# Optimization experiments

Hardware: AMD Instinct MI355X
Metric: run time of the kernel (lower is better)

## Reference

```python
import jax, jax.numpy as jnp
import numpy as np

S, B, H, F, E, K = 2048, 4, 1024, 4096, 8, 2


def setup_inputs() -> dict:
    key = jax.random.key(0)
    k1, k2, k3, k4 = jax.random.split(key, 4)
    scale_h = 1.0 / np.sqrt(H)
    scale_f = 1.0 / np.sqrt(F)
    return {
        "x": jax.random.normal(k1, (S, B, H), dtype=jnp.float32),
        "router_w": jax.random.normal(k2, (H, E), dtype=jnp.float32) * scale_h,
        "w1": jax.random.normal(k3, (E, H, F), dtype=jnp.float32) * scale_h,
        "w2": jax.random.normal(k4, (E, F, H), dtype=jnp.float32) * scale_f,
    }


def reference(x, router_w, w1, w2):
    # x: [S, B, H] (Megatron layout). Flatten to tokens.
    s, b, h = x.shape
    xt = x.reshape(-1, h)                       # [T, H], T = S*B
    # --- TopK router: softmax over expert logits, then top-k probs ---
    logits = xt @ router_w                      # [T, E]
    probs = jax.nn.softmax(logits, axis=-1)     # [T, E]
    top_p, top_i = jax.lax.top_k(probs, K)      # [T, K] each
    # --- Grouped-GEMM expert MLPs + weighted combine ---
    # Loop over the small fixed expert set; each expert applies fc1->gelu->fc2
    # to every token, masked/weighted by its routing probability (math is
    # identical to dispatch/permute/grouped-GEMM/combine in Megatron).
    out = jnp.zeros_like(xt)
    for e in range(E):
        gate_e = jnp.sum(jnp.where(top_i == e, top_p, 0.0), axis=-1)  # [T]
        hidden = jax.nn.gelu(xt @ w1[e], approximate=True)            # [T, F]
        out = out + gate_e[:, None] * (hidden @ w2[e])                # [T, H]
    return out.reshape(s, b, h)
```

## Files before the change

### kernel.cpp

```cpp
#include <hip/hip_runtime.h>
#include <cstdint>
#include <cstddef>

#define T_TOKENS 8192
#define H_DIM    1024
#define F_DIM    4096
#define E_NUM    8

typedef __bf16 bf16x8 __attribute__((ext_vector_type(8)));
typedef float  f32x4  __attribute__((ext_vector_type(4)));
typedef unsigned short ushort8 __attribute__((ext_vector_type(8)));

#define AS_GLOBAL(p) ((const __attribute__((address_space(1))) void*)(p))
#define AS_LDS(p)    ((__attribute__((address_space(3))) void*)(p))

__device__ inline unsigned short f2b(float f) {
  unsigned int u = __float_as_uint(f);
  unsigned int r = (u + 0x7fffu + ((u >> 16) & 1u)) >> 16;
  return (unsigned short)r;
}
__device__ inline float b2f(unsigned short u) {
  return __uint_as_float(((unsigned int)u) << 16);
}
__device__ inline float gelu_fast(float v) {
  float u2 = 1.5957691216057308f * v * (1.0f + 0.044715f * v * v);
  return v / (1.0f + __expf(-u2));
}

__global__ __launch_bounds__(256) void transpose_cast_kernel(
    const float* __restrict__ in, unsigned short* __restrict__ out, int R, int C)
{
  __shared__ float tile[64][65];
  const int e  = blockIdx.z;
  const int c0 = blockIdx.x * 64;
  const int r0 = blockIdx.y * 64;
  const float* src = in + (size_t)e * R * C;
  unsigned short* dst = out + (size_t)e * R * C;
  const int tid = threadIdx.x;
  const int rl  = tid >> 4;
  const int cl4 = (tid & 15) * 4;
#pragma unroll
  for (int i = 0; i < 4; ++i) {
    float4 v = *(const float4*)(src + (size_t)(r0 + rl + i * 16) * C + c0 + cl4);
    tile[rl + i * 16][cl4 + 0] = v.x;
    tile[rl + i * 16][cl4 + 1] = v.y;
    tile[rl + i * 16][cl4 + 2] = v.z;
    tile[rl + i * 16][cl4 + 3] = v.w;
  }
  __syncthreads();
  const int cl = tid >> 2;
  const int rb = (tid & 3) * 16;
#pragma unroll
  for (int j = 0; j < 4; ++j) {
    ushort4 u;
    u.x = f2b(tile[rb + j * 4 + 0][cl]);
    u.y = f2b(tile[rb + j * 4 + 1][cl]);
    u.z = f2b(tile[rb + j * 4 + 2][cl]);
    u.w = f2b(tile[rb + j * 4 + 3][cl]);
    *(ushort4*)(dst + (size_t)(c0 + cl) * R + r0 + rb + j * 4) = u;
  }
}

__global__ void zero_meta_kernel(int* __restrict__ counts) {
  if (threadIdx.x < 24) counts[threadIdx.x] = 0;
}

__global__ __launch_bounds__(256) void router_kernel(
    const float* __restrict__ x, const float* __restrict__ rw,
    unsigned short* __restrict__ xb, int* __restrict__ top_e, float* __restrict__ top_p,
    int* __restrict__ counts)
{
  __shared__ float lrw[H_DIM * 9];
  __shared__ int lc[E_NUM];
  const int tid = threadIdx.x;
  if (tid < E_NUM) lc[tid] = 0;
  for (int r = tid; r < H_DIM; r += 256) {
    const float* s = rw + r * 8;
    float4 a = *(const float4*)(s);
    float4 b = *(const float4*)(s + 4);
    float* d = &lrw[r * 9];
    d[0] = a.x; d[1] = a.y; d[2] = a.z; d[3] = a.w;
    d[4] = b.x; d[5] = b.y; d[6] = b.z; d[7] = b.w;
  }
  __syncthreads();
  const int lane = tid & 63, wid = tid >> 6;
  for (int i = 0; i < 8; ++i) {
    const int t = blockIdx.x * 32 + wid * 8 + i;
    float acc[8] = {0.f, 0.f, 0.f, 0.f, 0.f, 0.f, 0.f, 0.f};
    const float* xrow = x + (size_t)t * H_DIM;
    unsigned short* xbrow = xb + (size_t)t * H_DIM;
#pragma unroll
    for (int j = 0; j < 16; ++j) {
      int h = j * 64 + lane;
      float xv = xrow[h];
      xbrow[h] = f2b(xv);
      const float* rr = &lrw[h * 9];
#pragma unroll
      for (int e = 0; e < 8; ++e) acc[e] += xv * rr[e];
    }
#pragma unroll
    for (int e = 0; e < 8; ++e) {
#pragma unroll
      for (int s = 32; s > 0; s >>= 1) acc[e] += __shfl_xor(acc[e], s, 64);
    }
    if (lane == 0) {
      float mx = acc[0];
      for (int e = 1; e < 8; ++e) mx = fmaxf(mx, acc[e]);
      float p[8]; float sum = 0.f;
      for (int e = 0; e < 8; ++e) { p[e] = expf(acc[e] - mx); sum += p[e]; }
      float inv = 1.0f / sum;
      int i1 = 0; float b1 = p[0];
      for (int e = 1; e < 8; ++e) if (p[e] > b1) { b1 = p[e]; i1 = e; }
      int i2 = (i1 == 0) ? 1 : 0; float b2 = p[i2];
      for (int e = 0; e < 8; ++e) if (e != i1 && p[e] > b2) { b2 = p[e]; i2 = e; }
      top_e[2 * t]     = i1; top_p[2 * t]     = b1 * inv;
      top_e[2 * t + 1] = i2; top_p[2 * t + 1] = b2 * inv;
      atomicAdd(&lc[i1], 1);
      atomicAdd(&lc[i2], 1);
    }
  }
  __syncthreads();
  if (tid < E_NUM) atomicAdd(&counts[tid], lc[tid]);
}

__global__ void offsets_kernel(const int* __restrict__ counts,
                               int* __restrict__ offsets, int* __restrict__ cursor) {
  if (threadIdx.x == 0) {
    int o = 0;
    for (int e = 0; e < E_NUM; ++e) { offsets[e] = o; o += counts[e]; cursor[e] = 0; }
  }
}

__global__ __launch_bounds__(256) void assign_kernel(
    const int* __restrict__ top_e, const float* __restrict__ top_p,
    const int* __restrict__ offsets, int* __restrict__ cursor,
    int* __restrict__ map, float* __restrict__ gate, int* __restrict__ slot_of)
{
  __shared__ int lc[E_NUM], lb[E_NUM];
  const int tid = threadIdx.x;
  const int t = blockIdx.x * 256 + tid;
  if (tid < E_NUM) lc[tid] = 0;
  __syncthreads();
  int e0 = top_e[2 * t], e1 = top_e[2 * t + 1];
  int p0 = atomicAdd(&lc[e0], 1);
  int p1 = atomicAdd(&lc[e1], 1);
  __syncthreads();
  if (tid < E_NUM) lb[tid] = atomicAdd(&cursor[tid], lc[tid]);
  __syncthreads();
  int s0 = offsets[e0] + lb[e0] + p0;
  int s1 = offsets[e1] + lb[e1] + p1;
  map[s0] = t; gate[s0] = top_p[2 * t];
  map[s1] = t; gate[s1] = top_p[2 * t + 1];
  slot_of[2 * t] = s0; slot_of[2 * t + 1] = s1;
}

template <int KD, int ND, bool USE_MAP, bool GELU>
__global__ __launch_bounds__(256) void moe_gemm_kernel(
    const unsigned short* __restrict__ A, const unsigned short* __restrict__ Bt,
    const int* __restrict__ map, const float* __restrict__ gate,
    const int* __restrict__ counts, const int* __restrict__ offsets,
    unsigned short* __restrict__ C)
{
  __shared__ unsigned short ls[32768];
  const int e   = blockIdx.x;
  const int cnt = counts[e];
  const int tile_m = blockIdx.y;
  if (tile_m * 128 >= cnt) return;
  const int off    = offsets[e];
  const int tile_n = blockIdx.z;
  const int tid    = threadIdx.x;

  const unsigned short* aSrc[4];
  const unsigned short* bSrc[4];
  const int cswz = ((tid & 7) ^ ((tid >> 3) & 7)) * 8;
#pragma unroll
  for (int it = 0; it < 4; ++it) {
    int r  = it * 32 + (tid >> 3);
    int rm = tile_m * 128 + r;
    if (rm > cnt - 1) rm = cnt - 1;
    int arow = USE_MAP ? map[off + rm] : (off + rm);
    aSrc[it] = A + (size_t)arow * KD + cswz;
    int rn = tile_n * 128 + r;
    bSrc[it] = Bt + (size_t)e * ND * KD + (size_t)rn * KD + cswz;
  }

  const int lane = tid & 63;
  const int wid  = tid >> 6;
  const int wm = wid >> 1, wn = wid & 1;
  const int lr = lane & 15, kg = lane >> 4;
  const int swz = lr & 7;

  f32x4 acc[4][4];
#pragma unroll
  for (int mi = 0; mi < 4; ++mi)
#pragma unroll
    for (int ni = 0; ni < 4; ++ni) acc[mi][ni] = (f32x4){0.f, 0.f, 0.f, 0.f};

  constexpr int NK = KD / 64;

#pragma unroll
  for (int it = 0; it < 4; ++it)
    __builtin_amdgcn_global_load_lds(AS_GLOBAL(aSrc[it]),
                                     AS_LDS(ls + (it * 256 + tid) * 8), 16, 0, 0);
#pragma unroll
  for (int it = 0; it < 4; ++it)
    __builtin_amdgcn_global_load_lds(AS_GLOBAL(bSrc[it]),
                                     AS_LDS(ls + 16384 + (it * 256 + tid) * 8), 16, 0, 0);

#pragma unroll 1
  for (int k = 0; k < NK; ++k) {
    const int p = k & 1;
    asm volatile("s_barrier" ::: "memory");
    if (k + 1 < NK) {
      const int q = p ^ 1;
      const int k0 = (k + 1) * 64;
#pragma unroll
      for (int it = 0; it < 4; ++it)
        __builtin_amdgcn_global_load_lds(AS_GLOBAL(aSrc[it] + k0),
                                         AS_LDS(ls + q * 8192 + (it * 256 + tid) * 8), 16, 0, 0);
#pragma unroll
      for (int it = 0; it < 4; ++it)
        __builtin_amdgcn_global_load_lds(AS_GLOBAL(bSrc[it] + k0),
                                         AS_LDS(ls + 16384 + q * 8192 + (it * 256 + tid) * 8), 16, 0, 0);
      asm volatile("s_waitcnt vmcnt(8)" ::: "memory");
    } else {
      asm volatile("s_waitcnt vmcnt(0)" ::: "memory");
    }
    asm volatile("s_barrier" ::: "memory");

    const unsigned short* pA = ls + p * 8192 + (wm * 64 + lr) * 64;
    const unsigned short* pB = ls + 16384 + p * 8192 + (wn * 64 + lr) * 64;
#pragma unroll
    for (int ks = 0; ks < 2; ++ks) {
      bf16x8 aF[4], bF[4];
#pragma unroll
      for (int i = 0; i < 4; ++i)
        aF[i] = *(const bf16x8*)(pA + i * 16 * 64 + (((ks * 4 + kg) ^ swz) * 8));
#pragma unroll
      for (int i = 0; i < 4; ++i)
        bF[i] = *(const bf16x8*)(pB + i * 16 * 64 + (((ks * 4 + kg) ^ swz) * 8));
#pragma unroll
      for (int mi = 0; mi < 4; ++mi)
#pragma unroll
        for (int ni = 0; ni < 4; ++ni)
          acc[mi][ni] = __builtin_amdgcn_mfma_f32_16x16x32_bf16(aF[mi], bF[ni],
                                                                acc[mi][ni], 0, 0, 0);
    }
  }

  __syncthreads();
#pragma unroll
  for (int mi = 0; mi < 4; ++mi) {
#pragma unroll
    for (int r = 0; r < 4; ++r) {
      int Rl = wm * 64 + mi * 16 + kg * 4 + r;
      float gv = 1.0f;
      if (!GELU) {
        int gm = tile_m * 128 + Rl;
        int gmc = gm < cnt ? gm : cnt - 1;
        gv = gate[off + gmc];
      }
#pragma unroll
      for (int ni = 0; ni < 4; ++ni) {
        int col = wn * 64 + ni * 16 + lr;
        float v = acc[mi][ni][r];
        v = GELU ? gelu_fast(v) : v * gv;
        ls[Rl * 136 + col] = f2b(v);
      }
    }
  }
  __syncthreads();
#pragma unroll
  for (int it = 0; it < 8; ++it) {
    int g = it * 256 + tid;
    int R = g >> 4, c16 = g & 15;
    int gm = tile_m * 128 + R;
    if (gm < cnt) {
      ushort8 v = *(const ushort8*)(ls + R * 136 + c16 * 8);
      *(ushort8*)(C + (size_t)(off + gm) * ND + tile_n * 128 + c16 * 8) = v;
    }
  }
}

__global__ __launch_bounds__(256) void combine_kernel(
    const unsigned short* __restrict__ y, const int* __restrict__ slot_of,
    float* __restrict__ out)
{
  const int t  = blockIdx.x;
  const int h0 = threadIdx.x * 4;
  const int s0 = slot_of[2 * t], s1 = slot_of[2 * t + 1];
  ushort4 a = *(const ushort4*)(y + (size_t)s0 * H_DIM + h0);
  ushort4 b = *(const ushort4*)(y + (size_t)s1 * H_DIM + h0);
  float4 o;
  o.x = b2f(a.x) + b2f(b.x);
  o.y = b2f(a.y) + b2f(b.y);
  o.z = b2f(a.z) + b2f(b.z);
  o.w = b2f(a.w) + b2f(b.w);
  *(float4*)(out + (size_t)t * H_DIM + h0) = o;
}

extern "C" void kernel_launch(void* const* d_in, const int* in_sizes, int n_in,
                              void* d_out, int out_size, void* d_ws, size_t ws_size,
                              hipStream_t stream) {
  const float* x  = (const float*)d_in[0];
  const float* rw = (const float*)d_in[1];
  const float* w1 = (const float*)d_in[2];
  const float* w2 = (const float*)d_in[3];
  float* out = (float*)d_out;

  char* ws = (char*)d_ws;
  unsigned short* wT     = (unsigned short*)ws;
  unsigned short* xb     = (unsigned short*)(ws + (64ull  << 20));
  unsigned short* y      = (unsigned short*)(ws + (64ull  << 20));
  unsigned short* hidden = (unsigned short*)(ws + (96ull  << 20));
  char* meta = ws + (224ull << 20);
  int*   top_e   = (int*)meta;
  float* top_p   = (float*)(meta + (64 << 10));
  int*   map     = (int*)(meta + (128 << 10));
  float* gate    = (float*)(meta + (192 << 10));
  int*   slot_of = (int*)(meta + (256 << 10));
  int*   counts  = (int*)(meta + (320 << 10));
  int*   offsets = counts + 8;
  int*   cursor  = counts + 16;

  zero_meta_kernel<<<1, 64, 0, stream>>>(counts);
  transpose_cast_kernel<<<dim3(F_DIM / 64, H_DIM / 64, E_NUM), 256, 0, stream>>>(w1, wT, H_DIM, F_DIM);
  router_kernel<<<256, 256, 0, stream>>>(x, rw, xb, top_e, top_p, counts);
  offsets_kernel<<<1, 64, 0, stream>>>(counts, offsets, cursor);
  assign_kernel<<<T_TOKENS / 256, 256, 0, stream>>>(top_e, top_p, offsets, cursor, map, gate, slot_of);
  moe_gemm_kernel<H_DIM, F_DIM, true, true>
      <<<dim3(E_NUM, 64, F_DIM / 128), 256, 0, stream>>>(xb, wT, map, nullptr, counts, offsets, hidden);
  transpose_cast_kernel<<<dim3(H_DIM / 64, F_DIM / 64, E_NUM), 256, 0, stream>>>(w2, wT, F_DIM, H_DIM);
  moe_gemm_kernel<F_DIM, H_DIM, false, false>
      <<<dim3(E_NUM, 64, H_DIM / 128), 256, 0, stream>>>(hidden, wT, nullptr, gate, counts, offsets, y);
  combine_kernel<<<T_TOKENS, 256, 0, stream>>>(y, slot_of, out);
}
```

Before: 753.7 us.

## Add 256x256-tile 512-thread grouped GEMM for fc1 and widen transpose stores

Adds a new grouped GEMM kernel with 256x256 output tiles, 8 waves and double-buffered global-to-LDS loads, with priority hints around the MFMA phases. It is used only for the fc1 expert GEMM, to raise arithmetic intensity and cut reloads of the A and B tiles. Separately, the weight transpose-cast kernel now writes 8 bf16 values per store instead of 4. The larger tiles use much more LDS and many more accumulator registers, which lowers occupancy and wastes more padded rows when an expert's token count is not a multiple of 256.

```diff
diff --git a/kernel.cpp b/kernel.cpp
--- a/kernel.cpp
+++ b/kernel.cpp
@@ -48,16 +48,15 @@
     tile[rl + i * 16][cl4 + 3] = v.w;
   }
   __syncthreads();
-  const int cl = tid >> 2;
-  const int rb = (tid & 3) * 16;
-#pragma unroll
-  for (int j = 0; j < 4; ++j) {
-    ushort4 u;
-    u.x = f2b(tile[rb + j * 4 + 0][cl]);
-    u.y = f2b(tile[rb + j * 4 + 1][cl]);
-    u.z = f2b(tile[rb + j * 4 + 2][cl]);
-    u.w = f2b(tile[rb + j * 4 + 3][cl]);
-    *(ushort4*)(dst + (size_t)(c0 + cl) * R + r0 + rb + j * 4) = u;
+#pragma unroll
+  for (int itw = 0; itw < 2; ++itw) {
+    int g  = itw * 256 + tid;
+    int c  = g >> 3;
+    int rc = g & 7;
+    ushort8 u;
+#pragma unroll
+    for (int k = 0; k < 8; ++k) u[k] = f2b(tile[rc * 8 + k][c]);
+    *(ushort8*)(dst + (size_t)(c0 + c) * R + r0 + rc * 8) = u;
   }
 }
 
@@ -155,6 +154,178 @@
 }
 
 template <int KD, int ND, bool USE_MAP, bool GELU>
+__global__ __launch_bounds__(512, 2) void moe_gemm256_kernel(
+    const unsigned short* __restrict__ A, const unsigned short* __restrict__ Bt,
+    const int* __restrict__ map, const float* __restrict__ gate,
+    const int* __restrict__ counts, const int* __restrict__ offsets,
+    unsigned short* __restrict__ C)
+{
+  __shared__ unsigned short ls[65536];
+  const int e   = blockIdx.x;
+  const int cnt = counts[e];
+  const int tile_m = blockIdx.y;
+  if (tile_m * 256 >= cnt) return;
+  const int off    = offsets[e];
+  const int tile_n = blockIdx.z;
+  const int tid    = threadIdx.x;
+
+  const unsigned short* aSrc[4];
+  const unsigned short* bSrc[4];
+#pragma unroll
+  for (int it = 0; it < 4; ++it) {
+    int g   = it * 512 + tid;
+    int row = g >> 3;
+    int cs  = (g & 7) ^ (row & 7);
+    int rm  = tile_m * 256 + row;
+    if (rm > cnt - 1) rm = cnt - 1;
+    int arow = USE_MAP ? map[off + rm] : (off + rm);
+    aSrc[it] = A + (size_t)arow * KD + cs * 8;
+    int rn = tile_n * 256 + row;
+    bSrc[it] = Bt + (size_t)e * ND * KD + (size_t)rn * KD + cs * 8;
+  }
+
+  const int lane = tid & 63;
+  const int wid  = tid >> 6;
+  const int wm = wid >> 2, wn = wid & 3;
+  const int lr = lane & 15, kg = lane >> 4;
+  const int swz = lr & 7;
+
+  f32x4 acc[8][4];
+#pragma unroll
+  for (int mi = 0; mi < 8; ++mi)
+#pragma unroll
+    for (int ni = 0; ni < 4; ++ni) acc[mi][ni] = (f32x4){0.f, 0.f, 0.f, 0.f};
+
+  constexpr int NK = KD / 64;
+
+  auto STAGE = [&](int kt, int slot) {
+    const int kof = kt * 64;
+#pragma unroll
+    for (int it = 0; it < 4; ++it)
+      __builtin_amdgcn_global_load_lds(AS_GLOBAL(aSrc[it] + kof),
+          AS_LDS(ls + slot * 16384 + (it * 512 + tid) * 8), 16, 0, 0);
+#pragma unroll
+    for (int it = 0; it < 4; ++it)
+      __builtin_amdgcn_global_load_lds(AS_GLOBAL(bSrc[it] + kof),
+          AS_LDS(ls + 32768 + slot * 16384 + (it * 512 + tid) * 8), 16, 0, 0);
+  };
+
+  STAGE(0, 0);
+  STAGE(1, 1);
+  asm volatile("s_waitcnt vmcnt(8)" ::: "memory");
+  asm volatile("s_barrier" ::: "memory");
+
+#pragma unroll 1
+  for (int kt = 0; kt < NK; ++kt) {
+    const int s = kt & 1;
+    const unsigned short* pA = ls + s * 16384 + (wm * 128 + lr) * 64;
+    const unsigned short* pB = ls + 32768 + s * 16384 + (wn * 64 + lr) * 64;
+    bf16x8 aF[4], bF[4];
+
+#pragma unroll
+    for (int ni = 0; ni < 4; ++ni)
+      bF[ni] = *(const bf16x8*)(pB + ni * 16 * 64 + ((kg) ^ swz) * 8);
+#pragma unroll
+    for (int j = 0; j < 4; ++j)
+      aF[j] = *(const bf16x8*)(pA + j * 16 * 64 + ((kg) ^ swz) * 8);
+    asm volatile("s_barrier" ::: "memory");
+    __builtin_amdgcn_s_setprio(1);
+#pragma unroll
+    for (int j = 0; j < 4; ++j)
+#pragma unroll
+      for (int ni = 0; ni < 4; ++ni)
+        acc[j][ni] = __builtin_amdgcn_mfma_f32_16x16x32_bf16(aF[j], bF[ni], acc[j][ni], 0, 0, 0);
+    __builtin_amdgcn_s_setprio(0);
+
+#pragma unroll
+    for (int j = 0; j < 4; ++j)
+      aF[j] = *(const bf16x8*)(pA + (4 + j) * 16 * 64 + ((kg) ^ swz) * 8);
+    asm volatile("s_barrier" ::: "memory");
+    __builtin_amdgcn_s_setprio(1);
+#pragma unroll
+    for (int j = 0; j < 4; ++j)
+#pragma unroll
+      for (int ni = 0; ni < 4; ++ni)
+        acc[4 + j][ni] = __builtin_amdgcn_mfma_f32_16x16x32_bf16(aF[j], bF[ni], acc[4 + j][ni], 0, 0, 0);
+    __builtin_amdgcn_s_setprio(0);
+
+#pragma unroll
+    for (int ni = 0; ni < 4; ++ni)
+      bF[ni] = *(const bf16x8*)(pB + ni * 16 * 64 + ((4 + kg) ^ swz) * 8);
+#pragma unroll
+    for (int j = 0; j < 4; ++j)
+      aF[j] = *(const bf16x8*)(pA + j * 16 * 64 + ((4 + kg) ^ swz) * 8);
+    asm volatile("s_barrier" ::: "memory");
+    __builtin_amdgcn_s_setprio(1);
+#pragma unroll
+    for (int j = 0; j < 4; ++j)
+#pragma unroll
+      for (int ni = 0; ni < 4; ++ni)
+        acc[j][ni] = __builtin_amdgcn_mfma_f32_16x16x32_bf16(aF[j], bF[ni], acc[j][ni], 0, 0, 0);
+    __builtin_amdgcn_s_setprio(0);
+
+#pragma unroll
+    for (int j = 0; j < 4; ++j)
+      aF[j] = *(const bf16x8*)(pA + (4 + j) * 16 * 64 + ((4 + kg) ^ swz) * 8);
+    asm volatile("s_waitcnt lgkmcnt(0)" ::: "memory");
+    asm volatile("s_barrier" ::: "memory");
+    if (kt + 2 < NK) STAGE(kt + 2, s);
+    __builtin_amdgcn_s_setprio(1);
+#pragma unroll
+    for (int j = 0; j < 4; ++j)
+#pragma unroll
+      for (int ni = 0; ni < 4; ++ni)
+        acc[4 + j][ni] = __builtin_amdgcn_mfma_f32_16x16x32_bf16(aF[j], bF[ni], acc[4 + j][ni], 0, 0, 0);
+    __builtin_amdgcn_s_setprio(0);
+    if (kt + 2 < NK) {
+      asm volatile("s_waitcnt vmcnt(8)" ::: "memory");
+    } else {
+      asm volatile("s_waitcnt vmcnt(0)" ::: "memory");
+    }
+    asm volatile("s_barrier" ::: "memory");
+  }
+
+  __syncthreads();
+#pragma unroll
+  for (int h = 0; h < 2; ++h) {
+    if (h) __syncthreads();
+    if (wm == h) {
+#pragma unroll
+      for (int mi = 0; mi < 8; ++mi) {
+#pragma unroll
+        for (int r = 0; r < 4; ++r) {
+          int Rl = mi * 16 + kg * 4 + r;
+          float gv = 1.0f;
+          if (!GELU) {
+            int gm = tile_m * 256 + h * 128 + Rl;
+            int gmc = gm < cnt ? gm : cnt - 1;
+            gv = gate[off + gmc];
+          }
+#pragma unroll
+          for (int ni = 0; ni < 4; ++ni) {
+            int col = wn * 64 + ni * 16 + lr;
+            float v = acc[mi][ni][r];
+            v = GELU ? gelu_fast(v) : v * gv;
+            ls[Rl * 264 + col] = f2b(v);
+          }
+        }
+      }
+    }
+    __syncthreads();
+#pragma unroll
+    for (int it = 0; it < 8; ++it) {
+      int g = it * 512 + tid;
+      int R = g >> 5, c8 = g & 31;
+      int gm = tile_m * 256 + h * 128 + R;
+      if (gm < cnt) {
+        ushort8 v = *(const ushort8*)(ls + R * 264 + c8 * 8);
+        *(ushort8*)(C + (size_t)(off + gm) * ND + tile_n * 256 + c8 * 8) = v;
+      }
+    }
+  }
+}
+
+template <int KD, int ND, bool USE_MAP, bool GELU>
 __global__ __launch_bounds__(256) void moe_gemm_kernel(
     const unsigned short* __restrict__ A, const unsigned short* __restrict__ Bt,
     const int* __restrict__ map, const float* __restrict__ gate,
@@ -328,8 +499,8 @@
   router_kernel<<<256, 256, 0, stream>>>(x, rw, xb, top_e, top_p, counts);
   offsets_kernel<<<1, 64, 0, stream>>>(counts, offsets, cursor);
   assign_kernel<<<T_TOKENS / 256, 256, 0, stream>>>(top_e, top_p, offsets, cursor, map, gate, slot_of);
-  moe_gemm_kernel<H_DIM, F_DIM, true, true>
-      <<<dim3(E_NUM, 64, F_DIM / 128), 256, 0, stream>>>(xb, wT, map, nullptr, counts, offsets, hidden);
+  moe_gemm256_kernel<H_DIM, F_DIM, true, true>
+      <<<dim3(E_NUM, 32, F_DIM / 256), 512, 0, stream>>>(xb, wT, map, nullptr, counts, offsets, hidden);
   transpose_cast_kernel<<<dim3(H_DIM / 64, F_DIM / 64, E_NUM), 256, 0, stream>>>(w2, wT, F_DIM, H_DIM);
   moe_gemm_kernel<F_DIM, H_DIM, false, false>
       <<<dim3(E_NUM, 64, H_DIM / 128), 256, 0, stream>>>(hidden, wT, nullptr, gate, counts, offsets, y);
```

After: 796.9 us. 5.7% more time.

## Fuse combine into second GEMM via atomics and fold small setup kernels

Applied to the files above, without the earlier changes.

The second expert GEMM now scales its accumulators by the gate and atomically adds them in fp32 straight into the output rows, using the token map. This removes the bf16 intermediate y buffer and the separate combine kernel. To support this, the router kernel zeroes the output, the first transpose zeroes the counters, and assign computes the expert offsets itself, which drops two tiny launches. The transpose also writes 8-wide stores. In exchange the code relies on many scattered fp32 atomics and an extra full-size zeroing pass over the output.

```diff
diff --git a/kernel.cpp b/kernel.cpp
--- a/kernel.cpp
+++ b/kernel.cpp
@@ -28,15 +28,18 @@
 }
 
 __global__ __launch_bounds__(256) void transpose_cast_kernel(
-    const float* __restrict__ in, unsigned short* __restrict__ out, int R, int C)
+    const float* __restrict__ in, unsigned short* __restrict__ out, int R, int C,
+    int* __restrict__ zc)
 {
   __shared__ float tile[64][65];
+  const int tid = threadIdx.x;
+  if (zc && blockIdx.x == 0 && blockIdx.y == 0 && blockIdx.z == 0 && tid < 24)
+    zc[tid] = 0;
   const int e  = blockIdx.z;
   const int c0 = blockIdx.x * 64;
   const int r0 = blockIdx.y * 64;
   const float* src = in + (size_t)e * R * C;
   unsigned short* dst = out + (size_t)e * R * C;
-  const int tid = threadIdx.x;
   const int rl  = tid >> 4;
   const int cl4 = (tid & 15) * 4;
 #pragma unroll
@@ -48,31 +51,33 @@
     tile[rl + i * 16][cl4 + 3] = v.w;
   }
   __syncthreads();
-  const int cl = tid >> 2;
-  const int rb = (tid & 3) * 16;
-#pragma unroll
-  for (int j = 0; j < 4; ++j) {
-    ushort4 u;
-    u.x = f2b(tile[rb + j * 4 + 0][cl]);
-    u.y = f2b(tile[rb + j * 4 + 1][cl]);
-    u.z = f2b(tile[rb + j * 4 + 2][cl]);
-    u.w = f2b(tile[rb + j * 4 + 3][cl]);
-    *(ushort4*)(dst + (size_t)(c0 + cl) * R + r0 + rb + j * 4) = u;
-  }
-}
-
-__global__ void zero_meta_kernel(int* __restrict__ counts) {
-  if (threadIdx.x < 24) counts[threadIdx.x] = 0;
+#pragma unroll
+  for (int itw = 0; itw < 2; ++itw) {
+    int g  = itw * 256 + tid;
+    int c  = g >> 3;
+    int rc = g & 7;
+    ushort8 u;
+#pragma unroll
+    for (int k = 0; k < 8; ++k) u[k] = f2b(tile[rc * 8 + k][c]);
+    *(ushort8*)(dst + (size_t)(c0 + c) * R + r0 + rc * 8) = u;
+  }
 }
 
 __global__ __launch_bounds__(256) void router_kernel(
     const float* __restrict__ x, const float* __restrict__ rw,
     unsigned short* __restrict__ xb, int* __restrict__ top_e, float* __restrict__ top_p,
-    int* __restrict__ counts)
+    int* __restrict__ counts, float* __restrict__ out_zero)
 {
   __shared__ float lrw[H_DIM * 9];
   __shared__ int lc[E_NUM];
   const int tid = threadIdx.x;
+  {
+    float4 z = {0.f, 0.f, 0.f, 0.f};
+    float4* o4 = (float4*)out_zero;
+    int base = blockIdx.x * 256 + tid;
+#pragma unroll
+    for (int i = 0; i < 32; ++i) o4[base + i * 65536] = z;
+  }
   if (tid < E_NUM) lc[tid] = 0;
   for (int r = tid; r < H_DIM; r += 256) {
     const float* s = rw + r * 8;
@@ -123,23 +128,19 @@
   if (tid < E_NUM) atomicAdd(&counts[tid], lc[tid]);
 }
 
-__global__ void offsets_kernel(const int* __restrict__ counts,
-                               int* __restrict__ offsets, int* __restrict__ cursor) {
-  if (threadIdx.x == 0) {
-    int o = 0;
-    for (int e = 0; e < E_NUM; ++e) { offsets[e] = o; o += counts[e]; cursor[e] = 0; }
-  }
-}
-
 __global__ __launch_bounds__(256) void assign_kernel(
     const int* __restrict__ top_e, const float* __restrict__ top_p,
-    const int* __restrict__ offsets, int* __restrict__ cursor,
-    int* __restrict__ map, float* __restrict__ gate, int* __restrict__ slot_of)
+    const int* __restrict__ counts, int* __restrict__ cursor,
+    int* __restrict__ map, float* __restrict__ gate, int* __restrict__ offsets)
 {
-  __shared__ int lc[E_NUM], lb[E_NUM];
+  __shared__ int lc[E_NUM], lb[E_NUM], loff[E_NUM];
   const int tid = threadIdx.x;
   const int t = blockIdx.x * 256 + tid;
   if (tid < E_NUM) lc[tid] = 0;
+  if (tid == 0) {
+    int o = 0;
+    for (int e = 0; e < E_NUM; ++e) { loff[e] = o; o += counts[e]; }
+  }
   __syncthreads();
   int e0 = top_e[2 * t], e1 = top_e[2 * t + 1];
   int p0 = atomicAdd(&lc[e0], 1);
@@ -147,19 +148,19 @@
   __syncthreads();
   if (tid < E_NUM) lb[tid] = atomicAdd(&cursor[tid], lc[tid]);
   __syncthreads();
-  int s0 = offsets[e0] + lb[e0] + p0;
-  int s1 = offsets[e1] + lb[e1] + p1;
+  int s0 = loff[e0] + lb[e0] + p0;
+  int s1 = loff[e1] + lb[e1] + p1;
   map[s0] = t; gate[s0] = top_p[2 * t];
   map[s1] = t; gate[s1] = top_p[2 * t + 1];
-  slot_of[2 * t] = s0; slot_of[2 * t + 1] = s1;
-}
-
-template <int KD, int ND, bool USE_MAP, bool GELU>
+  if (blockIdx.x == 0 && tid < E_NUM) offsets[tid] = loff[tid];
+}
+
+template <int KD, int ND, bool USE_MAP, bool GELU, bool ATOMIC_OUT>
 __global__ __launch_bounds__(256) void moe_gemm_kernel(
     const unsigned short* __restrict__ A, const unsigned short* __restrict__ Bt,
     const int* __restrict__ map, const float* __restrict__ gate,
     const int* __restrict__ counts, const int* __restrict__ offsets,
-    unsigned short* __restrict__ C)
+    unsigned short* __restrict__ C, float* __restrict__ out)
 {
   __shared__ unsigned short ls[32768];
   const int e   = blockIdx.x;
@@ -248,55 +249,52 @@
     }
   }
 
-  __syncthreads();
-#pragma unroll
-  for (int mi = 0; mi < 4; ++mi) {
-#pragma unroll
-    for (int r = 0; r < 4; ++r) {
-      int Rl = wm * 64 + mi * 16 + kg * 4 + r;
-      float gv = 1.0f;
-      if (!GELU) {
+  if (ATOMIC_OUT) {
+#pragma unroll
+    for (int mi = 0; mi < 4; ++mi) {
+#pragma unroll
+      for (int r = 0; r < 4; ++r) {
+        int Rl = wm * 64 + mi * 16 + kg * 4 + r;
         int gm = tile_m * 128 + Rl;
-        int gmc = gm < cnt ? gm : cnt - 1;
-        gv = gate[off + gmc];
+        if (gm < cnt) {
+          int   t  = map[off + gm];
+          float gv = gate[off + gm];
+          float* orow = out + (size_t)t * ND + tile_n * 128 + wn * 64 + lr;
+#pragma unroll
+          for (int ni = 0; ni < 4; ++ni)
+            __hip_atomic_fetch_add(orow + ni * 16, acc[mi][ni][r] * gv,
+                                   __ATOMIC_RELAXED, __HIP_MEMORY_SCOPE_AGENT);
+        }
       }
-#pragma unroll
-      for (int ni = 0; ni < 4; ++ni) {
-        int col = wn * 64 + ni * 16 + lr;
-        float v = acc[mi][ni][r];
-        v = GELU ? gelu_fast(v) : v * gv;
-        ls[Rl * 136 + col] = f2b(v);
+    }
+  } else {
+    __syncthreads();
+#pragma unroll
+    for (int mi = 0; mi < 4; ++mi) {
+#pragma unroll
+      for (int r = 0; r < 4; ++r) {
+        int Rl = wm * 64 + mi * 16 + kg * 4 + r;
+#pragma unroll
+        for (int ni = 0; ni < 4; ++ni) {
+          int col = wn * 64 + ni * 16 + lr;
+          float v = acc[mi][ni][r];
+          v = GELU ? gelu_fast(v) : v;
+          ls[Rl * 136 + col] = f2b(v);
+        }
       }
     }
-  }
-  __syncthreads();
-#pragma unroll
-  for (int it = 0; it < 8; ++it) {
-    int g = it * 256 + tid;
-    int R = g >> 4, c16 = g & 15;
-    int gm = tile_m * 128 + R;
-    if (gm < cnt) {
-      ushort8 v = *(const ushort8*)(ls + R * 136 + c16 * 8);
-      *(ushort8*)(C + (size_t)(off + gm) * ND + tile_n * 128 + c16 * 8) = v;
-    }
-  }
-}
-
-__global__ __launch_bounds__(256) void combine_kernel(
-    const unsigned short* __restrict__ y, const int* __restrict__ slot_of,
-    float* __restrict__ out)
-{
-  const int t  = blockIdx.x;
-  const int h0 = threadIdx.x * 4;
-  const int s0 = slot_of[2 * t], s1 = slot_of[2 * t + 1];
-  ushort4 a = *(const ushort4*)(y + (size_t)s0 * H_DIM + h0);
-  ushort4 b = *(const ushort4*)(y + (size_t)s1 * H_DIM + h0);
-  float4 o;
-  o.x = b2f(a.x) + b2f(b.x);
-  o.y = b2f(a.y) + b2f(b.y);
-  o.z = b2f(a.z) + b2f(b.z);
-  o.w = b2f(a.w) + b2f(b.w);
-  *(float4*)(out + (size_t)t * H_DIM + h0) = o;
+    __syncthreads();
+#pragma unroll
+    for (int it = 0; it < 8; ++it) {
+      int g = it * 256 + tid;
+      int R = g >> 4, c16 = g & 15;
+      int gm = tile_m * 128 + R;
+      if (gm < cnt) {
+        ushort8 v = *(const ushort8*)(ls + R * 136 + c16 * 8);
+        *(ushort8*)(C + (size_t)(off + gm) * ND + tile_n * 128 + c16 * 8) = v;
+      }
+    }
+  }
 }
 
 extern "C" void kernel_launch(void* const* d_in, const int* in_sizes, int n_in,
@@ -311,27 +309,27 @@
   char* ws = (char*)d_ws;
   unsigned short* wT     = (unsigned short*)ws;
   unsigned short* xb     = (unsigned short*)(ws + (64ull  << 20));
-  unsigned short* y      = (unsigned short*)(ws + (64ull  << 20));
   unsigned short* hidden = (unsigned short*)(ws + (96ull  << 20));
   char* meta = ws + (224ull << 20);
   int*   top_e   = (int*)meta;
   float* top_p   = (float*)(meta + (64 << 10));
   int*   map     = (int*)(meta + (128 << 10));
   float* gate    = (float*)(meta + (192 << 10));
-  int*   slot_of = (int*)(meta + (256 << 10));
   int*   counts  = (int*)(meta + (320 << 10));
   int*   offsets = counts + 8;
   int*   cursor  = counts + 16;
 
-  zero_meta_kernel<<<1, 64, 0, stream>>>(counts);
-  transpose_cast_kernel<<<dim3(F_DIM / 64, H_DIM / 64, E_NUM), 256, 0, stream>>>(w1, wT, H_DIM, F_DIM);
-  router_kernel<<<256, 256, 0, stream>>>(x, rw, xb, top_e, top_p, counts);
-  offsets_kernel<<<1, 64, 0, stream>>>(counts, offsets, cursor);
-  assign_kernel<<<T_TOKENS / 256, 256, 0, stream>>>(top_e, top_p, offsets, cursor, map, gate, slot_of);
-  moe_gemm_kernel<H_DIM, F_DIM, true, true>
-      <<<dim3(E_NUM, 64, F_DIM / 128), 256, 0, stream>>>(xb, wT, map, nullptr, counts, offsets, hidden);
-  transpose_cast_kernel<<<dim3(H_DIM / 64, F_DIM / 64, E_NUM), 256, 0, stream>>>(w2, wT, F_DIM, H_DIM);
-  moe_gemm_kernel<F_DIM, H_DIM, false, false>
-      <<<dim3(E_NUM, 64, H_DIM / 128), 256, 0, stream>>>(hidden, wT, nullptr, gate, counts, offsets, y);
-  combine_kernel<<<T_TOKENS, 256, 0, stream>>>(y, slot_of, out);
-}
+  transpose_cast_kernel<<<dim3(F_DIM / 64, H_DIM / 64, E_NUM), 256, 0, stream>>>(
+      w1, wT, H_DIM, F_DIM, counts);
+  router_kernel<<<256, 256, 0, stream>>>(x, rw, xb, top_e, top_p, counts, out);
+  assign_kernel<<<T_TOKENS / 256, 256, 0, stream>>>(top_e, top_p, counts, cursor,
+                                                    map, gate, offsets);
+  moe_gemm_kernel<H_DIM, F_DIM, true, true, false>
+      <<<dim3(E_NUM, 64, F_DIM / 128), 256, 0, stream>>>(xb, wT, map, gate,
+                                                         counts, offsets, hidden, nullptr);
+  transpose_cast_kernel<<<dim3(H_DIM / 64, F_DIM / 64, E_NUM), 256, 0, stream>>>(
+      w2, wT, F_DIM, H_DIM, nullptr);
+  moe_gemm_kernel<F_DIM, H_DIM, false, false, true>
+      <<<dim3(E_NUM, 64, H_DIM / 128), 256, 0, stream>>>(hidden, wT, map, gate,
+                                                         counts, offsets, nullptr, out);
+}
```

New measurement: 765.1 us. Within noise of the previous version (+1.5%).
